# Performance work log

Hardware: AMD Instinct MI355X
Metric: run time of the kernel (lower is better)

The kernel has to match this reference:

```python
import jax, jax.numpy as jnp
import numpy as np

EPS = 1e-5
ROPE_BASE = 10000.0


def _layernorm(x, g, b):
    mu = jnp.mean(x, axis=-1, keepdims=True)
    var = jnp.mean(jnp.square(x - mu), axis=-1, keepdims=True)
    return (x - mu) * jax.lax.rsqrt(var + EPS) * g + b


def _rope(q, k):
    # q, k: (B, T, H, D); rotate interleaved pairs along last dim, positions over T
    T, D = q.shape[1], q.shape[-1]
    half = D // 2
    inv_freq = ROPE_BASE ** (-jnp.arange(half, dtype=jnp.float32) / half)
    ang = jnp.arange(T, dtype=jnp.float32)[:, None] * inv_freq  # (T, half)
    cos = jnp.cos(ang)[None, :, None, :]
    sin = jnp.sin(ang)[None, :, None, :]

    def rot(x):
        xr, xi = x[..., 0::2], x[..., 1::2]
        yr = xr * cos - xi * sin
        yi = xr * sin + xi * cos
        return jnp.stack([yr, yi], axis=-1).reshape(x.shape)

    return rot(q), rot(k)


def setup_inputs() -> dict:
    key = jax.random.key(0)
    ks = jax.random.split(key, 5)
    E, F, B, T = 1024, 4096, 2, 2048
    s = 0.02
    return {
        "x": jax.random.normal(ks[0], (B, T, E), jnp.float32),
        "in_proj_w": jax.random.normal(ks[1], (3 * E, E), jnp.float32) * s,
        "out_proj_w": jax.random.normal(ks[2], (E, E), jnp.float32) * s,
        "ln1_g": jnp.ones((E,), jnp.float32),
        "ln1_b": jnp.zeros((E,), jnp.float32),
        "ln2_g": jnp.ones((E,), jnp.float32),
        "ln2_b": jnp.zeros((E,), jnp.float32),
        "w1": jax.random.normal(ks[3], (F, E), jnp.float32) * s,
        "w2": jax.random.normal(ks[4], (E, F), jnp.float32) * s,
        "context": 256,
    }


def reference(x, in_proj_w, out_proj_w, ln1_g, ln1_b, ln2_g, ln2_b, w1, w2, context):
    B, T, E = x.shape
    H = 16
    D = E // H

    # ---- self-attention block (pre-norm, residual) ----
    h = _layernorm(x, ln1_g, ln1_b)
    proj = h @ in_proj_w.T  # (B, T, 3E)
    qkv = proj.reshape(B, T, 3, H, D)
    q = qkv[:, :, 0]  # (B, T, H, D)
    k = qkv[:, :, 1]
    v = qkv[:, :, 2].transpose(0, 2, 1, 3)  # (B, H, T, D)
    q, k = _rope(q, k)
    q = q.transpose(0, 2, 1, 3)  # (B, H, T, D)
    k = k.transpose(0, 2, 1, 3)

    pos = jnp.arange(T)
    delta = pos[:, None] - pos[None, :]  # (T, T)
    mask = (delta >= 0) & (delta < context)

    scores = jnp.einsum("bhtd,bhsd->bhts", q, k) / jnp.sqrt(jnp.float32(D))
    scores = jnp.where(mask[None, None], scores, jnp.float32(-1e30))
    attn = jax.nn.softmax(scores, axis=-1)
    o = jnp.einsum("bhts,bhsd->bhtd", attn, v)
    o = o.transpose(0, 2, 1, 3).reshape(B, T, E)
    x = x + o @ out_proj_w.T

    # ---- FFN block (pre-norm, residual) ----
    h = _layernorm(x, ln2_g, ln2_b)
    update = jax.nn.gelu(h @ w1.T, approximate=False) @ w2.T
    return x + update
```

## Files before the change

### kernel.cpp

```cpp
#include <hip/hip_runtime.h>
#include <math.h>

#define B_BATCH 2
#define T_SEQ   2048
#define E_DIM   1024
#define H_HEADS 16
#define D_HEAD  64
#define F_DIM   4096
#define M_ROWS  (B_BATCH * T_SEQ)

typedef __attribute__((ext_vector_type(8))) short short8;
typedef __attribute__((ext_vector_type(4))) float floatx4;
typedef __attribute__((ext_vector_type(8))) unsigned short ushortx8;

typedef __attribute__((address_space(1))) const void global_cvoid;
typedef __attribute__((address_space(3))) void lds_void;

__device__ __forceinline__ unsigned short f2bf(float f) {
    unsigned u = __float_as_uint(f);
    u += 0x7fffu + ((u >> 16) & 1u);
    return (unsigned short)(u >> 16);
}
__device__ __forceinline__ float bf2f(unsigned short h) {
    return __uint_as_float(((unsigned)h) << 16);
}

__device__ __forceinline__ float gelu_f(float v) {
    const float u = v * (0.7978845608f + 0.0356774081f * v * v);
    const float e = __expf(2.0f * u);
    const float t = 1.0f - 2.0f / (e + 1.0f);
    return 0.5f * v * (1.0f + t);
}

__device__ __forceinline__ float waveReduceSum(float v) {
#pragma unroll
    for (int off = 32; off > 0; off >>= 1) v += __shfl_xor(v, off, 64);
    return v;
}

__global__ __launch_bounds__(256) void cvt_all_kernel(const float* __restrict__ ipw,
                                                      const float* __restrict__ opw,
                                                      const float* __restrict__ w1,
                                                      const float* __restrict__ w2,
                                                      unsigned short* __restrict__ wqkv,
                                                      unsigned short* __restrict__ wout,
                                                      unsigned short* __restrict__ w1b,
                                                      unsigned short* __restrict__ w2b) {
    const size_t MEG = 1024u * 1024u;
    size_t i = ((size_t)blockIdx.x * 256 + threadIdx.x) * 4;
    const float* src;
    unsigned short* dst;
    size_t off;
    if (i < 3 * MEG)      { src = ipw; dst = wqkv; off = i; }
    else if (i < 4 * MEG) { src = opw; dst = wout; off = i - 3 * MEG; }
    else if (i < 8 * MEG) { src = w1;  dst = w1b;  off = i - 4 * MEG; }
    else                  { src = w2;  dst = w2b;  off = i - 8 * MEG; }
    float4 v = *(const float4*)(src + off);
    ushort4 o;
    o.x = f2bf(v.x); o.y = f2bf(v.y); o.z = f2bf(v.z); o.w = f2bf(v.w);
    *(ushort4*)(dst + off) = o;
}

__global__ __launch_bounds__(256) void reduce4_kernel(const float* __restrict__ p,
                                                      float* __restrict__ out, int n) {
    const int i = (blockIdx.x * 256 + threadIdx.x) * 4;
    if (i >= n) return;
    float4 a = *(const float4*)(out + i);
    float4 b0 = *(const float4*)(p + i);
    float4 b1 = *(const float4*)(p + (size_t)n + i);
    float4 b2 = *(const float4*)(p + 2 * (size_t)n + i);
    float4 b3 = *(const float4*)(p + 3 * (size_t)n + i);
    a.x += (b0.x + b1.x) + (b2.x + b3.x);
    a.y += (b0.y + b1.y) + (b2.y + b3.y);
    a.z += (b0.z + b1.z) + (b2.z + b3.z);
    a.w += (b0.w + b1.w) + (b2.w + b3.w);
    *(float4*)(out + i) = a;
}

__global__ __launch_bounds__(256) void rope_tab_kernel(float* __restrict__ tab) {
    const int idx = blockIdx.x * 256 + threadIdx.x;
    const int pos = idx >> 5, i = idx & 31;
    const float invf = powf(10000.0f, -(float)i / 32.0f);
    const float ang = (float)pos * invf;
    tab[idx * 2]     = cosf(ang);
    tab[idx * 2 + 1] = sinf(ang);
}

__global__ __launch_bounds__(256) void ln_kernel(const float* __restrict__ x,
                                                 const float* __restrict__ g,
                                                 const float* __restrict__ b,
                                                 unsigned short* __restrict__ out) {
    const int row = blockIdx.x;
    const float* xr = x + (size_t)row * E_DIM;
    float4 v = ((const float4*)xr)[threadIdx.x];
    float s  = v.x + v.y + v.z + v.w;
    float sq = v.x * v.x + v.y * v.y + v.z * v.z + v.w * v.w;

    __shared__ float red[8];
    float ws_ = waveReduceSum(s);
    float wq  = waveReduceSum(sq);
    int wid = threadIdx.x >> 6;
    if ((threadIdx.x & 63) == 0) { red[wid] = ws_; red[wid + 4] = wq; }
    __syncthreads();
    float ts = red[0] + red[1] + red[2] + red[3];
    float tq = red[4] + red[5] + red[6] + red[7];
    float mean = ts * (1.0f / E_DIM);
    float var  = tq * (1.0f / E_DIM) - mean * mean;
    float inv  = rsqrtf(var + 1e-5f);

    float4 gv = ((const float4*)g)[threadIdx.x];
    float4 bv = ((const float4*)b)[threadIdx.x];
    ushort4 o;
    o.x = f2bf((v.x - mean) * inv * gv.x + bv.x);
    o.y = f2bf((v.y - mean) * inv * gv.y + bv.y);
    o.z = f2bf((v.z - mean) * inv * gv.z + bv.z);
    o.w = f2bf((v.w - mean) * inv * gv.w + bv.w);
    ((ushort4*)(out + (size_t)row * E_DIM))[threadIdx.x] = o;
}

template <int EPI>
__global__ __launch_bounds__(256) void gemm_bf16(const unsigned short* __restrict__ A,
                                                 const unsigned short* __restrict__ Wt,
                                                 const float* __restrict__ R,
                                                 float* __restrict__ Cf,
                                                 unsigned short* __restrict__ Cb,
                                                 int M, int N, int K) {
    __shared__ unsigned short As[128 * 64];
    __shared__ unsigned short Bs[128 * 64];
    const int tid  = threadIdx.x;
    const int wave = tid >> 6, lane = tid & 63;
    const int wm   = wave >> 1, wn = wave & 1;
    const int quad = lane >> 4, l16 = lane & 15;
    const int m0 = blockIdx.y * 128, n0 = blockIdx.x * 128;
    const int Kc   = K / gridDim.z;
    const int kbeg = blockIdx.z * Kc;

    const int row_rel = lane >> 3;
    const int ch      = lane & 7;

    const floatx4 z = {0.0f, 0.0f, 0.0f, 0.0f};
    floatx4 acc[4][4];
#pragma unroll
    for (int i = 0; i < 4; ++i)
#pragma unroll
        for (int j = 0; j < 4; ++j) acc[i][j] = z;

    for (int k0 = kbeg; k0 < kbeg + Kc; k0 += 64) {
        __syncthreads();
#pragma unroll
        for (int i = 0; i < 4; ++i) {
            const int chunk = wave * 4 + i;
            const int grow  = chunk * 8 + row_rel;
            const int lch   = ch ^ (grow & 7);
            const unsigned short* ga = A  + (size_t)(m0 + grow) * K + k0 + lch * 8;
            const unsigned short* gb = Wt + (size_t)(n0 + grow) * K + k0 + lch * 8;
            __builtin_amdgcn_global_load_lds((global_cvoid*)ga,
                                             (lds_void*)(As + chunk * 512), 16, 0, 0);
            __builtin_amdgcn_global_load_lds((global_cvoid*)gb,
                                             (lds_void*)(Bs + chunk * 512), 16, 0, 0);
        }
        __syncthreads();

#pragma unroll
        for (int ks = 0; ks < 2; ++ks) {
            short8 af[4], bfr[4];
#pragma unroll
            for (int mt = 0; mt < 4; ++mt) {
                const int r = wm * 64 + mt * 16 + l16;
                const int p = (ks * 4 + quad) ^ (r & 7);
                af[mt] = *(const short8*)(As + r * 64 + p * 8);
            }
#pragma unroll
            for (int nt = 0; nt < 4; ++nt) {
                const int r = wn * 64 + nt * 16 + l16;
                const int p = (ks * 4 + quad) ^ (r & 7);
                bfr[nt] = *(const short8*)(Bs + r * 64 + p * 8);
            }
#pragma unroll
            for (int mt = 0; mt < 4; ++mt)
#pragma unroll
                for (int nt = 0; nt < 4; ++nt)
                    acc[mt][nt] = __builtin_amdgcn_mfma_f32_16x16x32_bf16(
                        af[mt], bfr[nt], acc[mt][nt], 0, 0, 0);
        }
    }

    const size_t zoff = (size_t)blockIdx.z * M * N;
#pragma unroll
    for (int mt = 0; mt < 4; ++mt) {
        const int rb = m0 + wm * 64 + mt * 16 + quad * 4;
#pragma unroll
        for (int nt = 0; nt < 4; ++nt) {
            const int col = n0 + wn * 64 + nt * 16 + l16;
#pragma unroll
            for (int r = 0; r < 4; ++r) {
                const size_t idx = (size_t)(rb + r) * N + col;
                const float v = acc[mt][nt][r];
                if (EPI == 0) {
                    Cf[idx] = v;
                } else if (EPI == 1) {
                    Cf[idx] = v + R[idx];
                } else if (EPI == 2) {
                    Cb[idx] = f2bf(gelu_f(v));
                } else if (EPI == 3) {
                    Cf[idx] += v;
                } else if (EPI == 4) {
                    Cb[idx] = f2bf(v);
                } else {
                    Cf[zoff + idx] = v;
                }
            }
        }
    }
}

__global__ __launch_bounds__(256) void vtrans_kernel(const unsigned short* __restrict__ proj,
                                                     unsigned short* __restrict__ vt) {
    __shared__ unsigned short L[64 * 72];
    const int bh = blockIdx.y, b = bh >> 4, h = bh & 15;
    const int st = blockIdx.x * 64;
    const int tid = threadIdx.x;
    {
        const int srel = tid >> 2, d16 = (tid & 3) * 16;
        const unsigned short* src =
            proj + (size_t)(b * T_SEQ + st + srel) * (3 * E_DIM) + 2 * E_DIM + h * 64 + d16;
        *(short8*)(L + srel * 72 + d16)     = *(const short8*)(src);
        *(short8*)(L + srel * 72 + d16 + 8) = *(const short8*)(src + 8);
    }
    __syncthreads();
    {
        const int d = tid >> 2, s16 = (tid & 3) * 16;
        short8 o0, o1;
#pragma unroll
        for (int j = 0; j < 8; ++j) {
            o0[j] = (short)L[(s16 + j) * 72 + d];
            o1[j] = (short)L[(s16 + 8 + j) * 72 + d];
        }
        unsigned short* dst = vt + (size_t)(bh * 64 + d) * T_SEQ + st + s16;
        *(short8*)dst       = o0;
        *(short8*)(dst + 8) = o1;
    }
}

__device__ __forceinline__ void rope16(ushortx8 x0, ushortx8 x1, const float* tp,
                                       short8& y0, short8& y1) {
#pragma unroll
    for (int j = 0; j < 4; ++j) {
        const float c = tp[2 * j], s = tp[2 * j + 1];
        const float xr = bf2f(x0[2 * j]), xi = bf2f(x0[2 * j + 1]);
        y0[2 * j]     = (short)f2bf(xr * c - xi * s);
        y0[2 * j + 1] = (short)f2bf(xr * s + xi * c);
    }
#pragma unroll
    for (int j = 0; j < 4; ++j) {
        const float c = tp[8 + 2 * j], s = tp[8 + 2 * j + 1];
        const float xr = bf2f(x1[2 * j]), xi = bf2f(x1[2 * j + 1]);
        y1[2 * j]     = (short)f2bf(xr * c - xi * s);
        y1[2 * j + 1] = (short)f2bf(xr * s + xi * c);
    }
}

__global__ __launch_bounds__(256) void attn_kernel(const unsigned short* __restrict__ proj,
                                                   const unsigned short* __restrict__ vt,
                                                   const float* __restrict__ tab,
                                                   const int* __restrict__ ctxp,
                                                   unsigned short* __restrict__ o) {
    __shared__ unsigned short Qs[64 * 64];
    __shared__ unsigned short Ks[64 * 64];
    __shared__ unsigned short Vs[64 * 64];
    __shared__ unsigned short Ps[4][16 * 64];

    const int ctx = ctxp[0];
    const int tid = threadIdx.x;
    const int wave = tid >> 6, lane = tid & 63;
    const int quad = lane >> 4, l16 = lane & 15;
    const int bh = blockIdx.y, b = bh >> 4, h = bh & 15;
    const int t0 = blockIdx.x * 64;

    {
        const int r = tid >> 2, d16 = (tid & 3) * 16;
        const int pos = t0 + r;
        const unsigned short* src =
            proj + (size_t)(b * T_SEQ + pos) * (3 * E_DIM) + h * 64 + d16;
        ushortx8 x0 = *(const ushortx8*)src;
        ushortx8 x1 = *(const ushortx8*)(src + 8);
        const float* tp = tab + ((size_t)pos * 32 + (d16 >> 1)) * 2;
        short8 y0, y1;
        rope16(x0, x1, tp, y0, y1);
        const int c0 = (tid & 3) * 2;
        *(short8*)(Qs + r * 64 + ((c0)     ^ (r & 7)) * 8) = y0;
        *(short8*)(Qs + r * 64 + ((c0 + 1) ^ (r & 7)) * 8) = y1;
    }

    int first = t0 - (ctx - 1);
    if (first < 0) first = 0;
    const int first_base = first & ~63;

    float m[4] = {-1e30f, -1e30f, -1e30f, -1e30f};
    float l[4] = {0.0f, 0.0f, 0.0f, 0.0f};
    const floatx4 z = {0.0f, 0.0f, 0.0f, 0.0f};
    floatx4 accO[4] = {z, z, z, z};

    const int q_row0 = t0 + wave * 16 + quad * 4;

    for (int s_base = first_base; s_base <= t0; s_base += 64) {
        __syncthreads();
        {
            const int r = tid >> 2, d16 = (tid & 3) * 16;
            const int pos = s_base + r;
            const unsigned short* src =
                proj + (size_t)(b * T_SEQ + pos) * (3 * E_DIM) + E_DIM + h * 64 + d16;
            ushortx8 x0 = *(const ushortx8*)src;
            ushortx8 x1 = *(const ushortx8*)(src + 8);
            const float* tp = tab + ((size_t)pos * 32 + (d16 >> 1)) * 2;
            short8 y0, y1;
            rope16(x0, x1, tp, y0, y1);
            const int c0 = (tid & 3) * 2;
            *(short8*)(Ks + r * 64 + ((c0)     ^ (r & 7)) * 8) = y0;
            *(short8*)(Ks + r * 64 + ((c0 + 1) ^ (r & 7)) * 8) = y1;
        }
#pragma unroll
        for (int i = 0; i < 2; ++i) {
            const int chunk = (wave * 2 + i) * 64 + lane;
            const int d = chunk >> 3, c = chunk & 7;
            const unsigned short* gsrc =
                vt + (size_t)(bh * 64 + d) * T_SEQ + s_base + ((c ^ (d & 7)) * 8);
            __builtin_amdgcn_global_load_lds((global_cvoid*)gsrc,
                                             (lds_void*)(Vs + (wave * 2 + i) * 512),
                                             16, 0, 0);
        }
        __syncthreads();

        floatx4 accS[4] = {z, z, z, z};
#pragma unroll
        for (int ks = 0; ks < 2; ++ks) {
            const int qrow = wave * 16 + l16;
            short8 aq = *(const short8*)(Qs + qrow * 64 + (((ks * 4 + quad) ^ (qrow & 7)) * 8));
#pragma unroll
            for (int nt = 0; nt < 4; ++nt) {
                const int kro = nt * 16 + l16;
                short8 bk = *(const short8*)(Ks + kro * 64 + (((ks * 4 + quad) ^ (kro & 7)) * 8));
                accS[nt] = __builtin_amdgcn_mfma_f32_16x16x32_bf16(aq, bk, accS[nt], 0, 0, 0);
            }
        }

        float p[4][4];
        float alpha[4];
#pragma unroll
        for (int r = 0; r < 4; ++r) {
            const int qa = q_row0 + r;
            float sv[4];
            float vmax = -1e30f;
#pragma unroll
            for (int nt = 0; nt < 4; ++nt) {
                const int sa = s_base + nt * 16 + l16;
                const int dd = qa - sa;
                const bool ok = (unsigned)dd < (unsigned)ctx;
                const float s = ok ? accS[nt][r] * 0.125f : -1e30f;
                sv[nt] = s;
                vmax = fmaxf(vmax, s);
            }
            vmax = fmaxf(vmax, __shfl_xor(vmax, 1));
            vmax = fmaxf(vmax, __shfl_xor(vmax, 2));
            vmax = fmaxf(vmax, __shfl_xor(vmax, 4));
            vmax = fmaxf(vmax, __shfl_xor(vmax, 8));
            const float mn = fmaxf(m[r], vmax);
            alpha[r] = __expf(m[r] - mn);
            float ps = 0.0f;
#pragma unroll
            for (int nt = 0; nt < 4; ++nt) {
                const float pe = (sv[nt] > -0.5e30f) ? __expf(sv[nt] - mn) : 0.0f;
                p[nt][r] = pe;
                ps += pe;
            }
            ps += __shfl_xor(ps, 1);
            ps += __shfl_xor(ps, 2);
            ps += __shfl_xor(ps, 4);
            ps += __shfl_xor(ps, 8);
            l[r] = l[r] * alpha[r] + ps;
            m[r] = mn;
        }

#pragma unroll
        for (int nt = 0; nt < 4; ++nt) {
#pragma unroll
            for (int r = 0; r < 4; ++r) {
                const int row = quad * 4 + r;
                const int col = nt * 16 + l16;
                Ps[wave][row * 64 + (((col >> 3) ^ (row & 7)) * 8) + (col & 7)] =
                    f2bf(p[nt][r]);
            }
        }
#pragma unroll
        for (int nt = 0; nt < 4; ++nt)
#pragma unroll
            for (int r = 0; r < 4; ++r) accO[nt][r] *= alpha[r];

#pragma unroll
        for (int ks = 0; ks < 2; ++ks) {
            short8 ap = *(const short8*)(&Ps[wave][l16 * 64 + (((ks * 4 + quad) ^ (l16 & 7)) * 8)]);
#pragma unroll
            for (int nt = 0; nt < 4; ++nt) {
                const int dr = nt * 16 + l16;
                short8 bv = *(const short8*)(Vs + dr * 64 + (((ks * 4 + quad) ^ (dr & 7)) * 8));
                accO[nt] = __builtin_amdgcn_mfma_f32_16x16x32_bf16(ap, bv, accO[nt], 0, 0, 0);
            }
        }
    }

    float inv[4];
#pragma unroll
    for (int r = 0; r < 4; ++r) inv[r] = 1.0f / l[r];
#pragma unroll
    for (int nt = 0; nt < 4; ++nt) {
#pragma unroll
        for (int r = 0; r < 4; ++r) {
            const int t = q_row0 + r;
            o[(size_t)(b * T_SEQ + t) * E_DIM + h * 64 + nt * 16 + l16] =
                f2bf(accO[nt][r] * inv[r]);
        }
    }
}

extern "C" void kernel_launch(void* const* d_in, const int* in_sizes, int n_in,
                              void* d_out, int out_size, void* d_ws, size_t ws_size,
                              hipStream_t stream) {
    const float* x          = (const float*)d_in[0];
    const float* in_proj_w  = (const float*)d_in[1];
    const float* out_proj_w = (const float*)d_in[2];
    const float* ln1_g      = (const float*)d_in[3];
    const float* ln1_b      = (const float*)d_in[4];
    const float* ln2_g      = (const float*)d_in[5];
    const float* ln2_b      = (const float*)d_in[6];
    const float* w1         = (const float*)d_in[7];
    const float* w2         = (const float*)d_in[8];
    const int*   ctx        = (const int*)d_in[9];
    float* out = (float*)d_out;
    float* ws  = (float*)d_ws;

    const size_t MEG = 1024u * 1024u;
    unsigned short* u = (unsigned short*)ws;
    unsigned short* w2_b   = u;
    unsigned short* wqkv_b = u + 4 * MEG;
    unsigned short* wout_b = u + 7 * MEG;
    unsigned short* w1_b   = u + 8 * MEG;
    unsigned short* h_b    = u + 12 * MEG;
    unsigned short* obuf_b = u + 16 * MEG;
    unsigned short* proj_b = u + 20 * MEG;
    unsigned short* vt_b   = u + 32 * MEG;
    unsigned short* mid_b  = u + 36 * MEG;
    float* tab  = ws + 26 * MEG;
    float* part = (float*)(u + 4 * MEG);

    cvt_all_kernel<<<12 * MEG / 1024, 256, 0, stream>>>(
        in_proj_w, out_proj_w, w1, w2, wqkv_b, wout_b, w1_b, w2_b);
    rope_tab_kernel<<<T_SEQ * 32 / 256, 256, 0, stream>>>(tab);

    ln_kernel<<<M_ROWS, 256, 0, stream>>>(x, ln1_g, ln1_b, h_b);
    gemm_bf16<4><<<dim3(3 * E_DIM / 128, M_ROWS / 128), 256, 0, stream>>>(
        h_b, wqkv_b, nullptr, nullptr, proj_b, M_ROWS, 3 * E_DIM, E_DIM);
    vtrans_kernel<<<dim3(T_SEQ / 64, B_BATCH * H_HEADS), 256, 0, stream>>>(proj_b, vt_b);
    attn_kernel<<<dim3(T_SEQ / 64, B_BATCH * H_HEADS), 256, 0, stream>>>(
        proj_b, vt_b, tab, ctx, obuf_b);
    gemm_bf16<1><<<dim3(E_DIM / 128, M_ROWS / 128), 256, 0, stream>>>(
        obuf_b, wout_b, x, out, nullptr, M_ROWS, E_DIM, E_DIM);
    ln_kernel<<<M_ROWS, 256, 0, stream>>>(out, ln2_g, ln2_b, h_b);
    gemm_bf16<2><<<dim3(F_DIM / 128, M_ROWS / 128), 256, 0, stream>>>(
        h_b, w1_b, nullptr, nullptr, mid_b, M_ROWS, F_DIM, E_DIM);
    gemm_bf16<5><<<dim3(E_DIM / 128, M_ROWS / 128, 4), 256, 0, stream>>>(
        mid_b, w2_b, nullptr, part, nullptr, M_ROWS, E_DIM, F_DIM);
    reduce4_kernel<<<M_ROWS * E_DIM / 1024, 256, 0, stream>>>(
        part, out, M_ROWS * E_DIM);
}
```

Baseline: 337.9 us.

## Remap GEMM blocks across XCDs, split-K out-proj, store partials as bf16

GEMM launches become 1D grids whose block IDs are remapped so that blocks landing on the same XCD (id&7) share M and N tiles, aiming for better L2 reuse. The output projection now uses 4-way split-K with a separate reduce kernel that adds the residual, which raises block count on a small GEMM. Split-K partials are stored as bf16 instead of fp32, halving partial-sum traffic but adding rounding error to the accumulated sums.

```diff
diff --git a/kernel.cpp b/kernel.cpp
--- a/kernel.cpp
+++ b/kernel.cpp
@@ -61,20 +61,38 @@
     *(ushort4*)(dst + off) = o;
 }
 
-__global__ __launch_bounds__(256) void reduce4_kernel(const float* __restrict__ p,
+template <bool HASR>
+__global__ __launch_bounds__(256) void reduce4_kernel(const unsigned short* __restrict__ p,
+                                                      const float* __restrict__ R,
                                                       float* __restrict__ out, int n) {
-    const int i = (blockIdx.x * 256 + threadIdx.x) * 4;
+    const int i = (blockIdx.x * 256 + threadIdx.x) * 8;
     if (i >= n) return;
-    float4 a = *(const float4*)(out + i);
-    float4 b0 = *(const float4*)(p + i);
-    float4 b1 = *(const float4*)(p + (size_t)n + i);
-    float4 b2 = *(const float4*)(p + 2 * (size_t)n + i);
-    float4 b3 = *(const float4*)(p + 3 * (size_t)n + i);
-    a.x += (b0.x + b1.x) + (b2.x + b3.x);
-    a.y += (b0.y + b1.y) + (b2.y + b3.y);
-    a.z += (b0.z + b1.z) + (b2.z + b3.z);
-    a.w += (b0.w + b1.w) + (b2.w + b3.w);
-    *(float4*)(out + i) = a;
+    ushortx8 a0 = *(const ushortx8*)(p + i);
+    ushortx8 a1 = *(const ushortx8*)(p + (size_t)n + i);
+    ushortx8 a2 = *(const ushortx8*)(p + 2 * (size_t)n + i);
+    ushortx8 a3 = *(const ushortx8*)(p + 3 * (size_t)n + i);
+    float base[8];
+    if (HASR) {
+        float4 r0 = *(const float4*)(R + i);
+        float4 r1 = *(const float4*)(R + i + 4);
+        base[0]=r0.x; base[1]=r0.y; base[2]=r0.z; base[3]=r0.w;
+        base[4]=r1.x; base[5]=r1.y; base[6]=r1.z; base[7]=r1.w;
+    } else {
+        float4 r0 = *(const float4*)(out + i);
+        float4 r1 = *(const float4*)(out + i + 4);
+        base[0]=r0.x; base[1]=r0.y; base[2]=r0.z; base[3]=r0.w;
+        base[4]=r1.x; base[5]=r1.y; base[6]=r1.z; base[7]=r1.w;
+    }
+    float4 o0, o1;
+    float* op = &o0.x;
+#pragma unroll
+    for (int j = 0; j < 8; ++j) {
+        float s = base[j] + (bf2f(a0[j]) + bf2f(a1[j])) + (bf2f(a2[j]) + bf2f(a3[j]));
+        if (j < 4) (&o0.x)[j] = s; else (&o1.x)[j - 4] = s;
+    }
+    (void)op;
+    *(float4*)(out + i)     = o0;
+    *(float4*)(out + i + 4) = o1;
 }
 
 __global__ __launch_bounds__(256) void rope_tab_kernel(float* __restrict__ tab) {
@@ -118,10 +136,9 @@
     ((ushort4*)(out + (size_t)row * E_DIM))[threadIdx.x] = o;
 }
 
-template <int EPI>
+template <int EPI, int Z>
 __global__ __launch_bounds__(256) void gemm_bf16(const unsigned short* __restrict__ A,
                                                  const unsigned short* __restrict__ Wt,
-                                                 const float* __restrict__ R,
                                                  float* __restrict__ Cf,
                                                  unsigned short* __restrict__ Cb,
                                                  int M, int N, int K) {
@@ -131,9 +148,21 @@
     const int wave = tid >> 6, lane = tid & 63;
     const int wm   = wave >> 1, wn = wave & 1;
     const int quad = lane >> 4, l16 = lane & 15;
-    const int m0 = blockIdx.y * 128, n0 = blockIdx.x * 128;
-    const int Kc   = K / gridDim.z;
-    const int kbeg = blockIdx.z * Kc;
+
+    const int id  = blockIdx.x;
+    const int xcd = id & 7, local = id >> 3;
+    const int mq  = M >> 9;
+    const int mt  = (xcd & 3) + 4 * (local % mq);
+    int nt_, zz;
+    if (Z == 1) {
+        zz  = 0;
+        nt_ = (xcd >> 2) + 2 * (local / mq);
+    } else {
+        zz  = (xcd >> 2) + 2 * ((local / mq) & 1);
+        nt_ = local / (mq * 2);
+    }
+    const int m0 = mt * 128, n0 = nt_ * 128;
+    const int Kc = K / Z, kbeg = zz * Kc;
 
     const int row_rel = lane >> 3;
     const int ch      = lane & 7;
@@ -165,49 +194,43 @@
         for (int ks = 0; ks < 2; ++ks) {
             short8 af[4], bfr[4];
 #pragma unroll
-            for (int mt = 0; mt < 4; ++mt) {
-                const int r = wm * 64 + mt * 16 + l16;
+            for (int mt2 = 0; mt2 < 4; ++mt2) {
+                const int r = wm * 64 + mt2 * 16 + l16;
                 const int p = (ks * 4 + quad) ^ (r & 7);
-                af[mt] = *(const short8*)(As + r * 64 + p * 8);
-            }
-#pragma unroll
-            for (int nt = 0; nt < 4; ++nt) {
-                const int r = wn * 64 + nt * 16 + l16;
+                af[mt2] = *(const short8*)(As + r * 64 + p * 8);
+            }
+#pragma unroll
+            for (int nt2 = 0; nt2 < 4; ++nt2) {
+                const int r = wn * 64 + nt2 * 16 + l16;
                 const int p = (ks * 4 + quad) ^ (r & 7);
-                bfr[nt] = *(const short8*)(Bs + r * 64 + p * 8);
-            }
-#pragma unroll
-            for (int mt = 0; mt < 4; ++mt)
-#pragma unroll
-                for (int nt = 0; nt < 4; ++nt)
-                    acc[mt][nt] = __builtin_amdgcn_mfma_f32_16x16x32_bf16(
-                        af[mt], bfr[nt], acc[mt][nt], 0, 0, 0);
-        }
-    }
-
-    const size_t zoff = (size_t)blockIdx.z * M * N;
-#pragma unroll
-    for (int mt = 0; mt < 4; ++mt) {
-        const int rb = m0 + wm * 64 + mt * 16 + quad * 4;
-#pragma unroll
-        for (int nt = 0; nt < 4; ++nt) {
-            const int col = n0 + wn * 64 + nt * 16 + l16;
+                bfr[nt2] = *(const short8*)(Bs + r * 64 + p * 8);
+            }
+#pragma unroll
+            for (int mt2 = 0; mt2 < 4; ++mt2)
+#pragma unroll
+                for (int nt2 = 0; nt2 < 4; ++nt2)
+                    acc[mt2][nt2] = __builtin_amdgcn_mfma_f32_16x16x32_bf16(
+                        af[mt2], bfr[nt2], acc[mt2][nt2], 0, 0, 0);
+        }
+    }
+
+    const size_t zoff = (size_t)zz * M * N;
+#pragma unroll
+    for (int mt2 = 0; mt2 < 4; ++mt2) {
+        const int rb = m0 + wm * 64 + mt2 * 16 + quad * 4;
+#pragma unroll
+        for (int nt2 = 0; nt2 < 4; ++nt2) {
+            const int col = n0 + wn * 64 + nt2 * 16 + l16;
 #pragma unroll
             for (int r = 0; r < 4; ++r) {
                 const size_t idx = (size_t)(rb + r) * N + col;
-                const float v = acc[mt][nt][r];
-                if (EPI == 0) {
-                    Cf[idx] = v;
-                } else if (EPI == 1) {
-                    Cf[idx] = v + R[idx];
-                } else if (EPI == 2) {
+                const float v = acc[mt2][nt2][r];
+                if (EPI == 2) {
                     Cb[idx] = f2bf(gelu_f(v));
-                } else if (EPI == 3) {
-                    Cf[idx] += v;
                 } else if (EPI == 4) {
                     Cb[idx] = f2bf(v);
                 } else {
-                    Cf[zoff + idx] = v;
+                    Cb[zoff + idx] = f2bf(v);
                 }
             }
         }
@@ -450,25 +473,28 @@
     unsigned short* vt_b   = u + 32 * MEG;
     unsigned short* mid_b  = u + 36 * MEG;
     float* tab  = ws + 26 * MEG;
-    float* part = (float*)(u + 4 * MEG);
+    unsigned short* part_op   = u + 20 * MEG;
+    unsigned short* part_mlp2 = u + 4 * MEG;
 
     cvt_all_kernel<<<12 * MEG / 1024, 256, 0, stream>>>(
         in_proj_w, out_proj_w, w1, w2, wqkv_b, wout_b, w1_b, w2_b);
     rope_tab_kernel<<<T_SEQ * 32 / 256, 256, 0, stream>>>(tab);
 
     ln_kernel<<<M_ROWS, 256, 0, stream>>>(x, ln1_g, ln1_b, h_b);
-    gemm_bf16<4><<<dim3(3 * E_DIM / 128, M_ROWS / 128), 256, 0, stream>>>(
-        h_b, wqkv_b, nullptr, nullptr, proj_b, M_ROWS, 3 * E_DIM, E_DIM);
+    gemm_bf16<4, 1><<<32 * 24, 256, 0, stream>>>(
+        h_b, wqkv_b, nullptr, proj_b, M_ROWS, 3 * E_DIM, E_DIM);
     vtrans_kernel<<<dim3(T_SEQ / 64, B_BATCH * H_HEADS), 256, 0, stream>>>(proj_b, vt_b);
     attn_kernel<<<dim3(T_SEQ / 64, B_BATCH * H_HEADS), 256, 0, stream>>>(
         proj_b, vt_b, tab, ctx, obuf_b);
-    gemm_bf16<1><<<dim3(E_DIM / 128, M_ROWS / 128), 256, 0, stream>>>(
-        obuf_b, wout_b, x, out, nullptr, M_ROWS, E_DIM, E_DIM);
+    gemm_bf16<5, 4><<<32 * 8 * 4, 256, 0, stream>>>(
+        obuf_b, wout_b, nullptr, part_op, M_ROWS, E_DIM, E_DIM);
+    reduce4_kernel<true><<<M_ROWS * E_DIM / 2048, 256, 0, stream>>>(
+        part_op, x, out, M_ROWS * E_DIM);
     ln_kernel<<<M_ROWS, 256, 0, stream>>>(out, ln2_g, ln2_b, h_b);
-    gemm_bf16<2><<<dim3(F_DIM / 128, M_ROWS / 128), 256, 0, stream>>>(
-        h_b, w1_b, nullptr, nullptr, mid_b, M_ROWS, F_DIM, E_DIM);
-    gemm_bf16<5><<<dim3(E_DIM / 128, M_ROWS / 128, 4), 256, 0, stream>>>(
-        mid_b, w2_b, nullptr, part, nullptr, M_ROWS, E_DIM, F_DIM);
-    reduce4_kernel<<<M_ROWS * E_DIM / 1024, 256, 0, stream>>>(
-        part, out, M_ROWS * E_DIM);
-}
+    gemm_bf16<2, 1><<<32 * 32, 256, 0, stream>>>(
+        h_b, w1_b, nullptr, mid_b, M_ROWS, F_DIM, E_DIM);
+    gemm_bf16<5, 4><<<32 * 8 * 4, 256, 0, stream>>>(
+        mid_b, w2_b, nullptr, part_mlp2, M_ROWS, E_DIM, F_DIM);
+    reduce4_kernel<false><<<M_ROWS * E_DIM / 2048, 256, 0, stream>>>(
+        part_mlp2, nullptr, out, M_ROWS * E_DIM);
+}
```

New measurement: 337.8 us. No clear change (-0.0%).
